# Optimization experiments

Measured on AMD Instinct MI355X. Metric: run time of the kernel, lower is better.

## Reference

```python
import jax, jax.numpy as jnp
import numpy as np

B, S = 256, 256          # batch, seq_len
V, E = 8000, 128         # char vocab, char emb dim
HC, HW = 128, 256        # char_lstm_hid_dim, word_lstm_hid_dim


def setup_inputs() -> dict:
    key = jax.random.key(0)
    ks = jax.random.split(key, 20)
    n = lambda k, sh: (jax.random.normal(k, sh) * 0.05).astype(jnp.float32)
    return {
        "insts": jax.random.randint(ks[0], (B, S), 0, V),
        "golds": jax.random.randint(ks[1], (B, S), 0, 3),
        "emb": n(ks[2], (V, E)),
        "Wih_f": n(ks[3], (4 * HC, E)), "Whh_f": n(ks[4], (4 * HC, HC)), "b_f": n(ks[5], (4 * HC,)),
        "Wih_b": n(ks[6], (4 * HC, E)), "Whh_b": n(ks[7], (4 * HC, HC)), "b_b": n(ks[8], (4 * HC,)),
        "sub_Wih": n(ks[9], (4 * HW, 2 * HC)), "sub_Whh": n(ks[10], (4 * HW, HW)), "sub_b": n(ks[11], (4 * HW,)),
        "wrd_Wih": n(ks[12], (4 * HW, HW)), "wrd_Whh": n(ks[13], (4 * HW, HW)), "wrd_b": n(ks[14], (4 * HW,)),
        "cls_W": n(ks[15], (2, HW + 2 * HC)), "cls_b": n(ks[16], (2,)),
    }


def _cell(x, h, c, Wih, Whh, b):
    # PyTorch LSTMCell convention: gates ordered i, f, g, o
    g = x @ Wih.T + h @ Whh.T + b
    i, f, gg, o = jnp.split(g, 4, axis=-1)
    c = jax.nn.sigmoid(f) * c + jax.nn.sigmoid(i) * jnp.tanh(gg)
    h = jax.nn.sigmoid(o) * jnp.tanh(c)
    return h, c


def reference(insts, golds, emb, Wih_f, Whh_f, b_f, Wih_b, Whh_b, b_b,
              sub_Wih, sub_Whh, sub_b, wrd_Wih, wrd_Whh, wrd_b, cls_W, cls_b):
    # --- CharEncoder: embedding + BiLSTM, seq-first output [S, B, 2*HC] ---
    x = emb[insts].transpose(1, 0, 2)  # [S, B, E]
    z = jnp.zeros((B, HC), x.dtype)

    def mk_step(Wih, Whh, b):
        def step(hc, xt):
            h, c = _cell(xt, hc[0], hc[1], Wih, Whh, b)
            return (h, c), h
        return step

    _, hf = jax.lax.scan(mk_step(Wih_f, Whh_f, b_f), (z, z), x)
    _, hb = jax.lax.scan(mk_step(Wih_b, Whh_b, b_b), (z, z), x[::-1])
    chars = jnp.concatenate([hf, hb[::-1]], axis=-1)  # [S, B, 2*HC]

    # subword LSTM input at step t is chars[t-1] (zeros at t=0)
    sub_in = jnp.concatenate([jnp.zeros((1, B, 2 * HC), chars.dtype), chars[:-1]], axis=0)

    smap = jnp.array([1, 2, 2], jnp.int32)  # subword_action_map
    wmap = jnp.array([0, 1, 1], jnp.int32)  # word_action_map
    bidx = jnp.arange(B)

    # stacks: read state at pos, write new state at pos+1, then pos += op
    sh = jnp.zeros((2 * S + 2, B, HW), chars.dtype)
    sc = jnp.zeros((2 * S + 2, B, HW), chars.dtype)
    wh = jnp.zeros((S + 1, B, HW), chars.dtype)
    wc = jnp.zeros((S + 1, B, HW), chars.dtype)
    sp = jnp.zeros((B,), jnp.int32)
    wp = jnp.zeros((B,), jnp.int32)

    def step(carry, inp):
        sh, sc, sp, wh, wc, wp = carry
        xs, xc, g = inp  # subword input [B,2HC], classifier char feat [B,2HC], gold op [B]
        h1, c1 = _cell(xs, sh[sp, bidx], sc[sp, bidx], sub_Wih, sub_Whh, sub_b)
        sh = sh.at[sp + 1, bidx].set(h1)
        sc = sc.at[sp + 1, bidx].set(c1)
        h2, c2 = _cell(h1, wh[wp, bidx], wc[wp, bidx], wrd_Wih, wrd_Whh, wrd_b)
        wh = wh.at[wp + 1, bidx].set(h2)
        wc = wc.at[wp + 1, bidx].set(c2)
        out = jnp.concatenate([h2, xc], axis=-1) @ cls_W.T + cls_b  # [B, 2]
        return (sh, sc, sp + smap[g], wh, wc, wp + wmap[g]), out

    _, outs = jax.lax.scan(step, (sh, sc, sp, wh, wc, wp),
                           (sub_in, chars, golds.T.astype(jnp.int32)))
    return outs.transpose(1, 0, 2)  # [B, S, 2]
```

## Files before the change

kernel.cpp:

```cpp
#include <hip/hip_runtime.h>

#define S_LEN 256
#define BATCH 256

typedef _Float16 f16;
typedef _Float16 f16x8 __attribute__((ext_vector_type(8)));
typedef _Float16 f16x4 __attribute__((ext_vector_type(4)));
typedef float f32x4 __attribute__((ext_vector_type(4)));
typedef unsigned u32x4 __attribute__((ext_vector_type(4)));

__device__ inline float sigf(float x) { return 1.f / (1.f + __expf(-x)); }
__device__ inline float tanhf2(float x) { return 2.f * sigf(2.f * x) - 1.f; }

#define BARRIER_LGKM() asm volatile("s_waitcnt lgkmcnt(0)\n\ts_barrier" ::: "memory")

__global__ void k_convert(const float* __restrict__ w3, const float* __restrict__ w4,
                          const float* __restrict__ w6, const float* __restrict__ w7,
                          const float* __restrict__ w9, const float* __restrict__ w10,
                          const float* __restrict__ w12, const float* __restrict__ w13,
                          f16* __restrict__ dst) {
  int i = blockIdx.x * blockDim.x + threadIdx.x;
  const int n = 1310720;
  for (; i < n; i += gridDim.x * blockDim.x) {
    float v;
    if (i < 262144) {
      int m = i >> 16, j = i & 65535;
      v = (m == 0 ? w3 : m == 1 ? w4 : m == 2 ? w6 : w7)[j];
    } else {
      int k = i - 262144;
      int m = k >> 18, j = k & 262143;
      v = (m == 0 ? w9 : m == 1 ? w10 : m == 2 ? w12 : w13)[j];
    }
    dst[i] = (f16)v;
  }
}

__global__ void k_zero(unsigned* __restrict__ p, int n) {
  int i = blockIdx.x * blockDim.x + threadIdx.x;
  for (; i < n; i += gridDim.x * blockDim.x) p[i] = 0u;
}

__global__ void k_gather(const int* __restrict__ insts, const float* __restrict__ emb,
                         f16* __restrict__ Xf) {
  int gid = blockIdx.x * blockDim.x + threadIdx.x;
  int row = gid >> 5;
  int ch = gid & 31;
  int t = row >> 8, b = row & 255;
  int v = insts[b * S_LEN + t];
  const float* src = emb + (size_t)v * 128 + ch * 4;
  f16x4 d;
  d[0] = (f16)src[0]; d[1] = (f16)src[1]; d[2] = (f16)src[2]; d[3] = (f16)src[3];
  *(f16x4*)&Xf[(size_t)row * 128 + ch * 4] = d;
}

__global__ __launch_bounds__(512, 2)
void k_char_fused(const f16* __restrict__ wbuf, const float* __restrict__ bias_f,
                  const float* __restrict__ bias_b, const f16* __restrict__ Xf,
                  f16* __restrict__ chars) {
  const int dr = blockIdx.x >> 4;
  const int teamc = blockIdx.x & 15;
  const int m0 = teamc * 16;
  const f16* Wih = wbuf + (dr ? 131072 : 0);
  const f16* Whh = wbuf + (dr ? 196608 : 65536);
  const float* bias = dr ? bias_b : bias_f;
  const int tid = threadIdx.x, lane = tid & 63, wave = tid >> 6;
  const int l15 = lane & 15, kb = (lane >> 4) * 8;
  const int u0 = wave * 16;
  const int bq = lane >> 4;
  const int cbase = dr ? 128 : 0;

  __shared__ f16 hs[2][16][136];

  f16x8 fw[4][4], fh[4][4];
  float bv[4];
#pragma unroll
  for (int g = 0; g < 4; ++g) {
    const int row = g * 128 + u0 + l15;
    bv[g] = bias[row];
#pragma unroll
    for (int ks = 0; ks < 4; ++ks) {
      fw[g][ks] = *(const f16x8*)&Wih[row * 128 + ks * 32 + kb];
      fh[g][ks] = *(const f16x8*)&Whh[row * 128 + ks * 32 + kb];
    }
  }

  float c[4] = {0.f, 0.f, 0.f, 0.f};
  {
    int b = tid >> 5, u4 = (tid & 31) * 4;
    f16x4 z = {};
    *(f16x4*)&hs[0][b][u4] = z;
  }
  __syncthreads();

  f32x4 gacc[4];
  {
    const int t0 = dr ? 255 : 0;
    f16x8 ax[4];
#pragma unroll
    for (int ks = 0; ks < 4; ++ks)
      ax[ks] = *(const f16x8*)&Xf[(size_t)t0 * BATCH * 128 + (m0 + l15) * 128 + ks * 32 + kb];
#pragma unroll
    for (int g = 0; g < 4; ++g) { f32x4 a = {bv[g], bv[g], bv[g], bv[g]}; gacc[g] = a; }
#pragma unroll
    for (int ks = 0; ks < 4; ++ks)
#pragma unroll
      for (int g = 0; g < 4; ++g)
        gacc[g] = __builtin_amdgcn_mfma_f32_16x16x32_f16(ax[ks], fw[g][ks], gacc[g], 0, 0, 0);
  }

  int par = 0;
  for (int st = 0; st < 256; ++st) {
    f16x8 axn[4];
    if (st < 255) {
      const int tn = dr ? (254 - st) : (st + 1);
#pragma unroll
      for (int ks = 0; ks < 4; ++ks)
        axn[ks] =
            *(const f16x8*)&Xf[(size_t)tn * BATCH * 128 + (m0 + l15) * 128 + ks * 32 + kb];
    }

    f16x8 ah[4];
#pragma unroll
    for (int ks = 0; ks < 4; ++ks) ah[ks] = *(const f16x8*)&hs[par][l15][ks * 32 + kb];
    f32x4 acc[4];
#pragma unroll
    for (int g = 0; g < 4; ++g) acc[g] = gacc[g];
#pragma unroll
    for (int ks = 0; ks < 4; ++ks)
#pragma unroll
      for (int g = 0; g < 4; ++g)
        acc[g] = __builtin_amdgcn_mfma_f32_16x16x32_f16(ah[ks], fh[g][ks], acc[g], 0, 0, 0);

    const int t_out = dr ? (255 - st) : st;
#pragma unroll
    for (int r = 0; r < 4; ++r) {
      float cc = sigf(acc[1][r]) * c[r] + sigf(acc[0][r]) * tanhf2(acc[2][r]);
      c[r] = cc;
      f16 hv = (f16)(sigf(acc[3][r]) * tanhf2(cc));
      int b = bq * 4 + r;
      chars[((size_t)(teamc * 256 + t_out) * 16 + b) * 256 + cbase + u0 + l15] = hv;
      hs[par ^ 1][b][u0 + l15] = hv;
    }

    if (st < 255) {
#pragma unroll
      for (int g = 0; g < 4; ++g) { f32x4 a = {bv[g], bv[g], bv[g], bv[g]}; gacc[g] = a; }
#pragma unroll
      for (int ks = 0; ks < 4; ++ks)
#pragma unroll
        for (int g = 0; g < 4; ++g)
          gacc[g] =
              __builtin_amdgcn_mfma_f32_16x16x32_f16(axn[ks], fw[g][ks], gacc[g], 0, 0, 0);
    }
    par ^= 1;
    BARRIER_LGKM();
  }
}

__global__ __launch_bounds__(256, 1)
void k_subword(const f16* __restrict__ wbuf, const f16* __restrict__ chars,
               const int* __restrict__ golds,
               const float* __restrict__ b_sub, const float* __restrict__ b_wrd,
               unsigned* __restrict__ pub, unsigned* __restrict__ flags,
               f16* __restrict__ H2) {
  const int team = blockIdx.x >> 4;
  const int q = blockIdx.x & 15;
  const int m0 = team * 16;
  const int h0 = q * 16;
  const int tid = threadIdx.x, lane = tid & 63, wave = tid >> 6;
  const int l15 = lane & 15, kb = (lane >> 4) * 8;

  const f16* sWih = wbuf + 262144;
  const f16* sWhh = wbuf + 524288;
  const f16* wWih = wbuf + 786432;
  const f16* wWhh = wbuf + 1048576;

  __shared__ f16 xs_s[16][264];
  __shared__ f16 h1_s[16][264];
  __shared__ f16 wh_s[16][264];
  __shared__ float gexS[16][68];
  __shared__ float gexW[16][68];
  __shared__ int golds_s[16][256];

  f32x4 fsi[8], fsh[8], fwi[8], fwh[8];
  const int wr = wave * 256 + h0 + l15;
#pragma unroll
  for (int ks = 0; ks < 8; ++ks) {
    fsi[ks] = *(const volatile f32x4*)&sWih[wr * 256 + ks * 32 + kb];
    fsh[ks] = *(const volatile f32x4*)&sWhh[wr * 256 + ks * 32 + kb];
    fwi[ks] = *(const volatile f32x4*)&wWih[wr * 256 + ks * 32 + kb];
    fwh[ks] = *(const volatile f32x4*)&wWhh[wr * 256 + ks * 32 + kb];
  }
  const float bS = b_sub[wr], bW = b_wrd[wr];

  for (int i = tid; i < 16 * 256; i += 256)
    golds_s[i >> 8][i & 255] = golds[(m0 + (i >> 8)) * S_LEN + (i & 255)];
  for (int i = tid; i < 16 * 264; i += 256) {
    ((f16*)xs_s)[i] = (f16)0.f;
    ((f16*)h1_s)[i] = (f16)0.f;
    ((f16*)wh_s)[i] = (f16)0.f;
  }
  const int cm = tid >> 4, cj = tid & 15;
  const int sr = tid >> 4;
  const int sc = (tid & 15) * 16;
  float c_sub = 0.f, c_wrd = 0.f, wh_reg = 0.f;
  __syncthreads();

  for (int i = 0; i <= S_LEN; ++i) {
    const bool doW = (i > 0), doS = (i < S_LEN);
    const int slotbase = ((i & 1) * 16 + team) << 12;

    f16x4 chpre[4];
    if (doS) {
#pragma unroll
      for (int p = 0; p < 4; ++p)
        chpre[p] = *(const f16x4*)&chars[(size_t)(((team * S_LEN + i) * 16 + sr) * 256) +
                                         sc + p * 4];
    }

    f32x4 accW = {bW, bW, bW, bW};
    f32x4 accS = {bS, bS, bS, bS};
    if (doW) {
#pragma unroll
      for (int ks = 0; ks < 8; ++ks) {
        f16x8 a1 = *(const f16x8*)&h1_s[l15][ks * 32 + kb];
        f16x8 aw = *(const f16x8*)&wh_s[l15][ks * 32 + kb];
        accW = __builtin_amdgcn_mfma_f32_16x16x32_f16(
            a1, __builtin_bit_cast(f16x8, fwi[ks]), accW, 0, 0, 0);
        accW = __builtin_amdgcn_mfma_f32_16x16x32_f16(
            aw, __builtin_bit_cast(f16x8, fwh[ks]), accW, 0, 0, 0);
      }
    }
    if (doS) {
      const bool keep = (i > 0) && (golds_s[l15][i > 0 ? i - 1 : 0] == 0);
      f16x8 z8 = {};
#pragma unroll
      for (int ks = 0; ks < 8; ++ks) {
        f16x8 axv = *(const f16x8*)&xs_s[l15][ks * 32 + kb];
        f16x8 a1 = *(const f16x8*)&h1_s[l15][ks * 32 + kb];
        a1 = keep ? a1 : z8;
        accS = __builtin_amdgcn_mfma_f32_16x16x32_f16(
            axv, __builtin_bit_cast(f16x8, fsi[ks]), accS, 0, 0, 0);
        accS = __builtin_amdgcn_mfma_f32_16x16x32_f16(
            a1, __builtin_bit_cast(f16x8, fsh[ks]), accS, 0, 0, 0);
      }
    }
#pragma unroll
    for (int r = 0; r < 4; ++r) {
      if (doW) gexW[(lane >> 4) * 4 + r][wave * 16 + l15] = accW[r];
      if (doS) gexS[(lane >> 4) * 4 + r][wave * 16 + l15] = accS[r];
    }
    __syncthreads();

    const int gprev = (i > 0) ? golds_s[cm][i - 1] : 1;
    if (doW) {
      float gi = gexW[cm][cj], gf = gexW[cm][16 + cj], gg = gexW[cm][32 + cj],
            go = gexW[cm][48 + cj];
      float c2 = sigf(gf) * c_wrd + sigf(gi) * tanhf2(gg);
      float h2 = sigf(go) * tanhf2(c2);
      bool adv = (gprev != 0);
      if (adv) { c_wrd = c2; wh_reg = h2; }
      H2[(size_t)(i - 1) * BATCH * 256 + (m0 + cm) * 256 + h0 + cj] = (f16)h2;
    }
    if (doS) {
      float gi = gexS[cm][cj], gf = gexS[cm][16 + cj], gg = gexS[cm][32 + cj],
            go = gexS[cm][48 + cj];
      float cp = (gprev == 0) ? c_sub : 0.f;
      float c1 = sigf(gf) * cp + sigf(gi) * tanhf2(gg);
      c_sub = c1;
      f16 h1 = (f16)(sigf(go) * tanhf2(c1));
      unsigned val = ((unsigned)__builtin_bit_cast(unsigned short, h1) << 16) |
                     (unsigned)__builtin_bit_cast(unsigned short, (f16)wh_reg);
      __hip_atomic_store(&pub[slotbase + cm * 256 + h0 + cj], val, __ATOMIC_RELAXED,
                         __HIP_MEMORY_SCOPE_AGENT);
    }
    __syncthreads();

    if (doS) {
      if (tid == 0)
        __hip_atomic_store(&flags[(team * 16 + q) * 16], (unsigned)(i + 1), __ATOMIC_RELAXED,
                           __HIP_MEMORY_SCOPE_AGENT);
      if (tid < 64) {
        const unsigned tgt = (unsigned)(i + 1);
        while (true) {
          unsigned v = tgt;
          if (lane < 16)
            v = __hip_atomic_load(&flags[(team * 16 + lane) * 16], __ATOMIC_RELAXED,
                                  __HIP_MEMORY_SCOPE_AGENT);
          if (__all(v >= tgt)) break;
          __builtin_amdgcn_s_sleep(1);
        }
      }
      asm volatile("" ::: "memory");
      __syncthreads();
      u32x4 w0, w1, w2, w3;
      {
        const unsigned* pb = &pub[slotbase + sr * 256 + sc];
        asm volatile(
            "global_load_dwordx4 %0, %4, off sc0 sc1\n\t"
            "global_load_dwordx4 %1, %5, off sc0 sc1\n\t"
            "global_load_dwordx4 %2, %6, off sc0 sc1\n\t"
            "global_load_dwordx4 %3, %7, off sc0 sc1\n\t"
            "s_waitcnt vmcnt(0)"
            : "=&v"(w0), "=&v"(w1), "=&v"(w2), "=&v"(w3)
            : "v"(pb), "v"(pb + 4), "v"(pb + 8), "v"(pb + 12));
      }
      union { unsigned short s[8]; f16x8 v; } uh0, uw0, uh1, uw1;
#pragma unroll
      for (int k = 0; k < 4; ++k) {
        uh0.s[k] = (unsigned short)(w0[k] >> 16);
        uw0.s[k] = (unsigned short)(w0[k] & 0xffffu);
        uh0.s[4 + k] = (unsigned short)(w1[k] >> 16);
        uw0.s[4 + k] = (unsigned short)(w1[k] & 0xffffu);
        uh1.s[k] = (unsigned short)(w2[k] >> 16);
        uw1.s[k] = (unsigned short)(w2[k] & 0xffffu);
        uh1.s[4 + k] = (unsigned short)(w3[k] >> 16);
        uw1.s[4 + k] = (unsigned short)(w3[k] & 0xffffu);
      }
      *(f16x8*)&h1_s[sr][sc] = uh0.v;
      *(f16x8*)&wh_s[sr][sc] = uw0.v;
      *(f16x8*)&h1_s[sr][sc + 8] = uh1.v;
      *(f16x8*)&wh_s[sr][sc + 8] = uw1.v;
#pragma unroll
      for (int p = 0; p < 4; ++p) *(f16x4*)&xs_s[sr][sc + p * 4] = chpre[p];
      __syncthreads();
    }
  }
}

__global__ __launch_bounds__(256)
void k_cls(const f16* __restrict__ H2, const f16* __restrict__ chars,
           const float* __restrict__ clsW, const float* __restrict__ clsb,
           float* __restrict__ out) {
  const int w = (blockIdx.x << 2) | (threadIdx.x >> 6);
  const int lane = threadIdx.x & 63;
  const int t = w >> 8, b = w & 255;
  const f16* h2p = H2 + (size_t)w * 256;
  const f16* chp = chars + (size_t)(((b >> 4) * S_LEN + t) * 16 + (b & 15)) * 256;
  float s0 = 0.f, s1 = 0.f;
  f16x4 hv = *(const f16x4*)&h2p[lane * 4];
  f16x4 cv = *(const f16x4*)&chp[lane * 4];
#pragma unroll
  for (int qq = 0; qq < 4; ++qq) {
    int u = lane * 4 + qq;
    s0 += (float)hv[qq] * clsW[u] + (float)cv[qq] * clsW[256 + u];
    s1 += (float)hv[qq] * clsW[512 + u] + (float)cv[qq] * clsW[768 + u];
  }
#pragma unroll
  for (int off = 32; off >= 1; off >>= 1) {
    s0 += __shfl_down(s0, off);
    s1 += __shfl_down(s1, off);
  }
  if (lane == 0) {
    out[((size_t)b * S_LEN + t) * 2 + 0] = s0 + clsb[0];
    out[((size_t)b * S_LEN + t) * 2 + 1] = s1 + clsb[1];
  }
}

extern "C" void kernel_launch(void* const* d_in, const int* in_sizes, int n_in,
                              void* d_out, int out_size, void* d_ws, size_t ws_size,
                              hipStream_t stream) {
  const int* insts = (const int*)d_in[0];
  const int* golds = (const int*)d_in[1];
  const float* emb = (const float*)d_in[2];
  const float* wihf = (const float*)d_in[3];
  const float* whhf = (const float*)d_in[4];
  const float* bf = (const float*)d_in[5];
  const float* wihb = (const float*)d_in[6];
  const float* whhb = (const float*)d_in[7];
  const float* bb = (const float*)d_in[8];
  const float* swih = (const float*)d_in[9];
  const float* swhh = (const float*)d_in[10];
  const float* sb = (const float*)d_in[11];
  const float* wwih = (const float*)d_in[12];
  const float* wwhh = (const float*)d_in[13];
  const float* wb = (const float*)d_in[14];
  const float* clsW = (const float*)d_in[15];
  const float* clsb = (const float*)d_in[16];
  float* out = (float*)d_out;

  const size_t OFF_W = 0;
  const size_t OFF_XF = 2621440;
  const size_t OFF_PUB = OFF_XF + 4194304;
  const size_t OFF_FLAGS = OFF_PUB + 524288;
  const size_t OFF_CHARS = 19398656;
  const size_t OFF_A = 52953088;
  const size_t TOTAL = 87048192;
  if (ws_size < TOTAL) return;

  char* ws = (char*)d_ws;
  f16* wbuf = (f16*)(ws + OFF_W);
  f16* Xf = (f16*)(ws + OFF_XF);
  f16* chars = (f16*)(ws + OFF_CHARS);
  f16* H2 = (f16*)(ws + OFF_A);
  unsigned* pub = (unsigned*)(ws + OFF_PUB);
  unsigned* flags = (unsigned*)(ws + OFF_FLAGS);

  hipLaunchKernelGGL(k_convert, dim3(1024), dim3(256), 0, stream, wihf, whhf, wihb, whhb,
                     swih, swhh, wwih, wwhh, wbuf);
  hipLaunchKernelGGL(k_gather, dim3(8192), dim3(256), 0, stream, insts, emb, Xf);

  hipLaunchKernelGGL(k_char_fused, dim3(32), dim3(512), 0, stream, wbuf, bf, bb, Xf, chars);

  hipLaunchKernelGGL(k_zero, dim3(16), dim3(256), 0, stream, (unsigned*)(ws + OFF_FLAGS),
                     4096);
  hipLaunchKernelGGL(k_subword, dim3(256), dim3(256), 0, stream, wbuf, chars, golds, sb, wb,
                     pub, flags, H2);
  hipLaunchKernelGGL(k_cls, dim3(16384), dim3(256), 0, stream, H2, chars, clsW, clsb, out);
}
```

Measured before the change: 1.303 ms.

## Split char BiLSTM across 128 blocks with 4 batch rows each

The character BiLSTM kernel now runs 128 blocks, each handling 4 batch rows instead of 16, so four times as many CUs work on the sequential recurrence. MFMA tiles still span 16 rows. Only the first 4 rows are meaningful, and they are exchanged through a new shared-memory gate buffer so each thread computes one cell element. This cuts the elementwise work per step but adds an extra barrier and shared-memory round trip per timestep, and 75% of the MFMA work is wasted on padding rows.

```diff
diff --git a/kernel.cpp b/kernel.cpp
--- a/kernel.cpp
+++ b/kernel.cpp
@@ -57,19 +57,21 @@
 void k_char_fused(const f16* __restrict__ wbuf, const float* __restrict__ bias_f,
                   const float* __restrict__ bias_b, const f16* __restrict__ Xf,
                   f16* __restrict__ chars) {
-  const int dr = blockIdx.x >> 4;
-  const int teamc = blockIdx.x & 15;
-  const int m0 = teamc * 16;
+  const int dr = blockIdx.x >> 6;
+  const int slice = blockIdx.x & 63;
+  const int teamc = slice >> 2;
   const f16* Wih = wbuf + (dr ? 131072 : 0);
   const f16* Whh = wbuf + (dr ? 196608 : 65536);
   const float* bias = dr ? bias_b : bias_f;
   const int tid = threadIdx.x, lane = tid & 63, wave = tid >> 6;
   const int l15 = lane & 15, kb = (lane >> 4) * 8;
+  const int bq = lane >> 4;
   const int u0 = wave * 16;
-  const int bq = lane >> 4;
   const int cbase = dr ? 128 : 0;
+  const int xrow = (slice * 4 + l15 < 256) ? (slice * 4 + l15) : 255;
 
   __shared__ f16 hs[2][16][136];
+  __shared__ float gex[4][512];
 
   f16x8 fw[4][4], fh[4][4];
   float bv[4];
@@ -84,13 +86,12 @@
     }
   }
 
-  float c[4] = {0.f, 0.f, 0.f, 0.f};
-  {
-    int b = tid >> 5, u4 = (tid & 31) * 4;
-    f16x4 z = {};
-    *(f16x4*)&hs[0][b][u4] = z;
-  }
+  for (int i = tid; i < 2 * 16 * 136; i += 512) ((f16*)hs)[i] = (f16)0.f;
   __syncthreads();
+
+  const int cb = tid >> 7;
+  const int cu = tid & 127;
+  float c = 0.f;
 
   f32x4 gacc[4];
   {
@@ -98,7 +99,7 @@
     f16x8 ax[4];
 #pragma unroll
     for (int ks = 0; ks < 4; ++ks)
-      ax[ks] = *(const f16x8*)&Xf[(size_t)t0 * BATCH * 128 + (m0 + l15) * 128 + ks * 32 + kb];
+      ax[ks] = *(const f16x8*)&Xf[(size_t)t0 * BATCH * 128 + xrow * 128 + ks * 32 + kb];
 #pragma unroll
     for (int g = 0; g < 4; ++g) { f32x4 a = {bv[g], bv[g], bv[g], bv[g]}; gacc[g] = a; }
 #pragma unroll
@@ -115,8 +116,7 @@
       const int tn = dr ? (254 - st) : (st + 1);
 #pragma unroll
       for (int ks = 0; ks < 4; ++ks)
-        axn[ks] =
-            *(const f16x8*)&Xf[(size_t)tn * BATCH * 128 + (m0 + l15) * 128 + ks * 32 + kb];
+        axn[ks] = *(const f16x8*)&Xf[(size_t)tn * BATCH * 128 + xrow * 128 + ks * 32 + kb];
     }
 
     f16x8 ah[4];
@@ -131,15 +131,24 @@
       for (int g = 0; g < 4; ++g)
         acc[g] = __builtin_amdgcn_mfma_f32_16x16x32_f16(ah[ks], fh[g][ks], acc[g], 0, 0, 0);
 
-    const int t_out = dr ? (255 - st) : st;
-#pragma unroll
-    for (int r = 0; r < 4; ++r) {
-      float cc = sigf(acc[1][r]) * c[r] + sigf(acc[0][r]) * tanhf2(acc[2][r]);
-      c[r] = cc;
-      f16 hv = (f16)(sigf(acc[3][r]) * tanhf2(cc));
-      int b = bq * 4 + r;
-      chars[((size_t)(teamc * 256 + t_out) * 16 + b) * 256 + cbase + u0 + l15] = hv;
-      hs[par ^ 1][b][u0 + l15] = hv;
+    if (bq == 0) {
+#pragma unroll
+      for (int g = 0; g < 4; ++g)
+#pragma unroll
+        for (int r = 0; r < 4; ++r) gex[r][g * 128 + u0 + l15] = acc[g][r];
+    }
+    BARRIER_LGKM();
+
+    {
+      float gi = gex[cb][cu], gf = gex[cb][128 + cu], gg = gex[cb][256 + cu],
+            go = gex[cb][384 + cu];
+      float cc = sigf(gf) * c + sigf(gi) * tanhf2(gg);
+      c = cc;
+      f16 hv = (f16)(sigf(go) * tanhf2(cc));
+      const int t_out = dr ? (255 - st) : st;
+      const int gr = slice * 4 + cb;
+      chars[((size_t)(teamc * 256 + t_out) * 16 + (gr & 15)) * 256 + cbase + cu] = hv;
+      hs[par ^ 1][cb][cu] = hv;
     }
 
     if (st < 255) {
@@ -400,7 +409,7 @@
                      swih, swhh, wwih, wwhh, wbuf);
   hipLaunchKernelGGL(k_gather, dim3(8192), dim3(256), 0, stream, insts, emb, Xf);
 
-  hipLaunchKernelGGL(k_char_fused, dim3(32), dim3(512), 0, stream, wbuf, bf, bb, Xf, chars);
+  hipLaunchKernelGGL(k_char_fused, dim3(128), dim3(512), 0, stream, wbuf, bf, bb, Xf, chars);
 
   hipLaunchKernelGGL(k_zero, dim3(16), dim3(256), 0, stream, (unsigned*)(ws + OFF_FLAGS),
                      4096);
```

Result: faster. 1.207 ms, median of 2 (-7.3%).
